# Optimization experiments

Measured on AMD Instinct MI355X. Metric: run time of the kernel, lower is better.

## Reference

```python
import jax, jax.numpy as jnp
import numpy as np

B, T, E, H = 2, 2048, 1024, 16
D = E // H  # head_dim = 64


def setup_inputs() -> dict:
    key = jax.random.key(0)
    kx, kq, kk, kv, ko = jax.random.split(key, 5)
    x = jax.random.normal(kx, (B, T, E), dtype=jnp.float32)
    # nn.Parameter(torch.randn(...)) -> standard normal params
    Wq = jax.random.normal(kq, (H, E, D), dtype=jnp.float32)
    Wk = jax.random.normal(kk, (H, E, D), dtype=jnp.float32)
    Wv = jax.random.normal(kv, (H, E, D), dtype=jnp.float32)
    # nn.Linear(E, E, bias=False): weight [out, in], y = a @ Wo.T
    Wo = jax.random.normal(ko, (E, E), dtype=jnp.float32) * (1.0 / np.sqrt(E))
    # boolean mask: True positions are filled with -inf (causal: strict upper tri)
    mask = jnp.triu(jnp.ones((T, T), dtype=bool), k=1)
    return {"x": x, "mask": mask, "Wq": Wq, "Wk": Wk, "Wv": Wv, "Wo": Wo}


def reference(x, mask, Wq, Wk, Wv, Wo):
    # x: [b, t, e]; Wq/Wk/Wv: [h, e, i]
    q = jnp.einsum('hei,bte->hbti', Wq, x)
    k = jnp.einsum('hei,bte->hbti', Wk, x)
    v = jnp.einsum('hei,bte->hbti', Wv, x)
    # NOTE: original scales by sqrt(seq_len) (x.shape[1]), not sqrt(head_dim)
    scale = x.shape[1] ** 0.5
    fit = jnp.einsum('hbti,hbTi->hbtT', q, k) / scale  # [h, b, t, T]
    fit = jnp.where(mask, -jnp.inf, fit)
    p = jax.nn.softmax(fit, axis=-1)
    att = jnp.einsum('hbtT,hbTi->hbti', p, v)          # [h, b, t, i]
    # rearrange 'h b t i -> b t (h i)'
    b, t = att.shape[1], att.shape[2]
    att = jnp.transpose(att, (1, 2, 0, 3)).reshape(b, t, -1)
    return att @ Wo.T
```

## Files before the change

kernel.cpp:

```cpp
#include <hip/hip_runtime.h>
#include <hip/hip_fp8.h>
#include <stdint.h>

constexpr float INV_SCALE = 0.022097086912079608f;
constexpr float LOG2E = 1.4426950408889634f;
constexpr float QSC = INV_SCALE * LOG2E;

typedef __attribute__((ext_vector_type(8))) short bfrag;
typedef __attribute__((ext_vector_type(4))) float facc;
typedef __attribute__((ext_vector_type(4))) unsigned short us4;

#define MFMA(a, b, c) __builtin_amdgcn_mfma_f32_16x16x32_bf16((a), (b), (c), 0, 0, 0)
#define EXP2(x) __builtin_amdgcn_exp2f(x)

__device__ __forceinline__ unsigned short f2bh(float f) {
    union { float f; unsigned int u; } cv; cv.f = f;
    unsigned int u = cv.u;
    u += 0x7FFFu + ((u >> 16) & 1u);
    return (unsigned short)(u >> 16);
}
__device__ __forceinline__ float bh2f(unsigned short h) {
    union { unsigned int u; float f; } cv; cv.u = ((unsigned int)h) << 16;
    return cv.f;
}
__device__ __forceinline__ void gl_lds16(const unsigned short* g, unsigned short* lds) {
    __builtin_amdgcn_global_load_lds(
        (const __attribute__((address_space(1))) unsigned int*)g,
        (__attribute__((address_space(3))) unsigned int*)lds, 16, 0, 0);
}
__device__ __forceinline__ bfrag f8frag(uint2 raw) {
    union { uint2 u; unsigned char b[8]; } cv; cv.u = raw;
    bfrag r;
    #pragma unroll
    for (int j = 0; j < 8; ++j) {
        const __hip_fp8_e4m3* t = reinterpret_cast<const __hip_fp8_e4m3*>(&cv.b[j]);
        r[j] = (short)f2bh((float)(*t) * 0.00390625f);
    }
    return r;
}

__global__ __launch_bounds__(256) void prep_xw(const float* __restrict__ x,
                                               const float* __restrict__ Wo,
                                               unsigned short* __restrict__ xh,
                                               unsigned short* __restrict__ xl,
                                               unsigned short* __restrict__ WoB) {
    if (blockIdx.x < 1024) {
        int idx = blockIdx.x * 256 + threadIdx.x;
        facc v = *(const facc*)&Wo[(size_t)idx * 4];
        us4 o;
        #pragma unroll
        for (int j = 0; j < 4; ++j) o[j] = f2bh(v[j]);
        *(us4*)&WoB[(size_t)idx * 4] = o;
    } else {
        int idx = (blockIdx.x - 1024) * 256 + threadIdx.x;
        facc v = *(const facc*)&x[(size_t)idx * 4];
        us4 hv, lv;
        #pragma unroll
        for (int j = 0; j < 4; ++j) {
            unsigned short hb = f2bh(v[j]);
            hv[j] = hb;
            lv[j] = f2bh(v[j] - bh2f(hb));
        }
        *(us4*)&xh[(size_t)idx * 4] = hv;
        *(us4*)&xl[(size_t)idx * 4] = lv;
    }
}

__global__ __launch_bounds__(256) void prep_w(
    const float* __restrict__ Wq, const float* __restrict__ Wk, const float* __restrict__ Wv,
    unsigned short* __restrict__ WqTh, unsigned short* __restrict__ WqTl,
    unsigned short* __restrict__ WkTh, unsigned short* __restrict__ WkTl,
    unsigned short* __restrict__ WvT)
{
    __shared__ float tile[64][65];
    const int tid = threadIdx.x;
    const int et = blockIdx.x, h = blockIdx.y, m = blockIdx.z;
    const float* W = (m == 0) ? Wq : (m == 1) ? Wk : Wv;
    #pragma unroll
    for (int rep = 0; rep < 4; ++rep) {
        int idx = rep * 256 + tid;
        int e = idx >> 4, i4 = (idx & 15) * 4;
        facc v = *(const facc*)&W[(size_t)h * 65536 + (size_t)(et * 64 + e) * 64 + i4];
        tile[e][i4] = v.x; tile[e][i4 + 1] = v.y; tile[e][i4 + 2] = v.z; tile[e][i4 + 3] = v.w;
    }
    __syncthreads();
    unsigned short* Oh = (m == 0) ? WqTh : (m == 1) ? WkTh : WvT;
    unsigned short* Ol = (m == 0) ? WqTl : WkTl;
    #pragma unroll
    for (int rep = 0; rep < 4; ++rep) {
        int idx = rep * 256 + tid;
        int i = idx >> 4, e4 = (idx & 15) * 4;
        us4 hv, lv;
        #pragma unroll
        for (int j = 0; j < 4; ++j) {
            float f = tile[e4 + j][i];
            unsigned short hb = f2bh(f);
            hv[j] = hb;
            lv[j] = f2bh(f - bh2f(hb));
        }
        size_t o = (size_t)(h * 64 + i) * 1024 + et * 64 + e4;
        *(us4*)&Oh[o] = hv;
        if (m < 2) *(us4*)&Ol[o] = lv;
    }
}

__global__ __launch_bounds__(512, 2) void qkv_fused(
    const unsigned short* __restrict__ xh, const unsigned short* __restrict__ xl,
    const unsigned short* __restrict__ WqTh, const unsigned short* __restrict__ WqTl,
    const unsigned short* __restrict__ WkTh, const unsigned short* __restrict__ WkTl,
    const unsigned short* __restrict__ WvT,
    unsigned short* __restrict__ qh, unsigned char* __restrict__ ql8,
    unsigned short* __restrict__ kh, unsigned short* __restrict__ kl,
    unsigned short* __restrict__ vT)
{
    extern __shared__ unsigned short sm[];
    unsigned short* Ab = sm;
    unsigned short* Qb = sm + 16384;
    unsigned short* Kb = sm + 32768;
    unsigned short* Vb = sm + 49152;
    const int tid = threadIdx.x;
    const int w = tid >> 6, l = tid & 63;
    const int wm = w >> 2, wn = w & 3;
    const int ct = blockIdx.x, rt = blockIdx.y;

    const int lc = (l & 7) ^ (l >> 3);
    const int krel = (lc & 3) * 8;
    const unsigned short* Axp = (lc < 4) ? xh : xl;
    const unsigned short* Qp  = (lc < 4) ? WqTh : WqTl;
    const unsigned short* Kp  = (lc < 4) ? WkTh : WkTl;

    facc accq[4][2], acck[4][2], accv[4][2];
    #pragma unroll
    for (int m = 0; m < 4; ++m)
        #pragma unroll
        for (int n = 0; n < 2; ++n) {
            accq[m][n] = (facc)(0.0f); acck[m][n] = (facc)(0.0f); accv[m][n] = (facc)(0.0f);
        }

    auto stageAB = [&](int buf, int e0) {
        #pragma unroll
        for (int i = 0; i < 2; ++i) {
            int slice = w * 2 + i;
            int row = slice * 8 + (l >> 3);
            size_t sa = (size_t)(rt * 128 + row) * 1024 + e0 + krel;
            size_t sb = (size_t)(ct * 128 + row) * 1024 + e0 + krel;
            gl_lds16(&Axp[sa], &Ab[buf * 8192 + slice * 512]);
            gl_lds16(&Qp[sb],  &Qb[buf * 8192 + slice * 512]);
            gl_lds16(&Kp[sb],  &Kb[buf * 8192 + slice * 512]);
        }
    };

    stageAB(0, 0);
    #pragma unroll
    for (int i = 0; i < 2; ++i) {
        int slice = w * 2 + i;
        int row = slice * 8 + (l >> 3);
        gl_lds16(&WvT[(size_t)(ct * 128 + row) * 1024 + lc * 8], &Vb[slice * 512]);
    }
    asm volatile("s_waitcnt vmcnt(0)" ::: "memory");
    __builtin_amdgcn_s_barrier();

    for (int t = 0; t < 32; ++t) {
        __builtin_amdgcn_s_barrier();
        __builtin_amdgcn_sched_barrier(0);
        if (t < 31) stageAB((t + 1) & 1, (t + 1) * 32);
        {
            int wv = (t >> 1) + 1;
            if (wv < 16) {
                int slice = w + (t & 1) * 8;
                int row = slice * 8 + (l >> 3);
                gl_lds16(&WvT[(size_t)(ct * 128 + row) * 1024 + wv * 64 + lc * 8],
                         &Vb[(wv & 1) * 8192 + slice * 512]);
            }
        }
        __builtin_amdgcn_sched_barrier(0);
        if (t < 30)       asm volatile("s_waitcnt vmcnt(7)" ::: "memory");
        else if (t == 30) asm volatile("s_waitcnt vmcnt(6)" ::: "memory");
        else              asm volatile("s_waitcnt vmcnt(0)" ::: "memory");
        __builtin_amdgcn_sched_barrier(0);
        __builtin_amdgcn_s_barrier();
        __builtin_amdgcn_sched_barrier(0);

        const unsigned short* Ac = &Ab[(t & 1) * 8192];
        const unsigned short* Qc = &Qb[(t & 1) * 8192];
        const unsigned short* Kc = &Kb[(t & 1) * 8192];
        const unsigned short* Vc = &Vb[((t >> 1) & 1) * 8192];
        const int ca = (l >> 4) ^ (l & 7);
        const int cb = ca ^ 4;
        const int cv = ca ^ ((t & 1) << 2);

        bfrag afh[4], afl[4];
        #pragma unroll
        for (int m = 0; m < 4; ++m) {
            int row = wm * 64 + m * 16 + (l & 15);
            afh[m] = *(const bfrag*)&Ac[row * 64 + ca * 8];
            afl[m] = *(const bfrag*)&Ac[row * 64 + cb * 8];
        }
        #pragma unroll
        for (int n = 0; n < 2; ++n) {
            int nr = wn * 32 + n * 16 + (l & 15);
            bfrag bv = *(const bfrag*)&Vc[nr * 64 + cv * 8];
            #pragma unroll
            for (int m = 0; m < 4; ++m) accv[m][n] = MFMA(afh[m], bv, accv[m][n]);
        }
        #pragma unroll
        for (int n = 0; n < 2; ++n) {
            int nr = wn * 32 + n * 16 + (l & 15);
            bfrag bh = *(const bfrag*)&Qc[nr * 64 + ca * 8];
            bfrag bl = *(const bfrag*)&Qc[nr * 64 + cb * 8];
            #pragma unroll
            for (int m = 0; m < 4; ++m) {
                accq[m][n] = MFMA(afh[m], bh, accq[m][n]);
                accq[m][n] = MFMA(afh[m], bl, accq[m][n]);
                accq[m][n] = MFMA(afl[m], bh, accq[m][n]);
            }
        }
        #pragma unroll
        for (int n = 0; n < 2; ++n) {
            int nr = wn * 32 + n * 16 + (l & 15);
            bfrag bh = *(const bfrag*)&Kc[nr * 64 + ca * 8];
            bfrag bl = *(const bfrag*)&Kc[nr * 64 + cb * 8];
            #pragma unroll
            for (int m = 0; m < 4; ++m) {
                acck[m][n] = MFMA(afh[m], bh, acck[m][n]);
                acck[m][n] = MFMA(afh[m], bl, acck[m][n]);
                acck[m][n] = MFMA(afl[m], bh, acck[m][n]);
            }
        }
    }

    #pragma unroll
    for (int m = 0; m < 4; ++m)
        #pragma unroll
        for (int r = 0; r < 4; ++r) {
            int row = rt * 128 + wm * 64 + m * 16 + (l >> 4) * 4 + r;
            #pragma unroll
            for (int n = 0; n < 2; ++n) {
                int col = ct * 128 + wn * 32 + n * 16 + (l & 15);
                float fq = accq[m][n][r] * QSC;
                unsigned short hb = f2bh(fq);
                qh[(size_t)row * 1024 + col] = hb;
                __hip_fp8_e4m3 e((fq - bh2f(hb)) * 256.0f);
                ql8[(size_t)row * 1024 + col] = *reinterpret_cast<unsigned char*>(&e);
                float fk = acck[m][n][r];
                unsigned short kb = f2bh(fk);
                kh[(size_t)row * 1024 + col] = kb;
                kl[(size_t)row * 1024 + col] = f2bh(fk - bh2f(kb));
            }
        }
    #pragma unroll
    for (int m = 0; m < 4; ++m) {
        int t0g = rt * 128 + wm * 64 + m * 16 + (l >> 4) * 4;
        int b_ = t0g >> 11, t0 = t0g & 2047;
        #pragma unroll
        for (int n = 0; n < 2; ++n) {
            int col = ct * 128 + wn * 32 + n * 16 + (l & 15);
            int h_ = col >> 6, d = col & 63;
            us4 pk;
            #pragma unroll
            for (int r = 0; r < 4; ++r) pk[r] = f2bh(accv[m][n][r]);
            *(us4*)&vT[((size_t)((h_ * 2 + b_) * 64 + d)) * 2048 + t0] = pk;
        }
    }
}

__device__ __forceinline__ void stage_kv(
    const unsigned short* __restrict__ kh, const unsigned short* __restrict__ kl,
    const unsigned short* __restrict__ vT,
    unsigned short* Khb, unsigned short* Klb, unsigned short* Vtb,
    int w, int l, int b, int h, int kt)
{
    #pragma unroll
    for (int i = 0; i < 2; ++i) {
        int pbase = (w * 2 + i) * 1024;
        int p = pbase + l * 16;
        int row = p >> 7, slot = (p >> 4) & 7;
        int chunk = slot ^ (row & 7);
        size_t srcK = (size_t)(b * 2048 + kt * 64 + row) * 1024 + h * 64 + chunk * 8;
        size_t srcV = ((size_t)(h * 2 + b) * 64 + row) * 2048 + (size_t)kt * 64 + chunk * 8;
        gl_lds16(&kh[srcK], &Khb[pbase >> 1]);
        gl_lds16(&kl[srcK], &Klb[pbase >> 1]);
        gl_lds16(&vT[srcV], &Vtb[pbase >> 1]);
    }
}

__device__ __forceinline__ void causal_mask(facc* S, int w, int l) {
    #pragma unroll
    for (int f = 0; f < 4; ++f) {
        int keyl = f * 16 + (l & 15);
        #pragma unroll
        for (int r = 0; r < 4; ++r) {
            int qls = w * 16 + (l >> 4) * 4 + r;
            if (keyl > qls) S[f][r] = -1e30f;
        }
    }
}

__device__ __forceinline__ void softmax_pw(
    facc* S, float* mrow, float* lrow, facc* O,
    unsigned short* Pl, int w, int l)
{
    float mx[4];
    float dmax = -3.0e38f;
    #pragma unroll
    for (int r = 0; r < 4; ++r) {
        float m0 = fmaxf(fmaxf(S[0][r], S[1][r]), fmaxf(S[2][r], S[3][r]));
        m0 = fmaxf(m0, __shfl_xor(m0, 1));
        m0 = fmaxf(m0, __shfl_xor(m0, 2));
        m0 = fmaxf(m0, __shfl_xor(m0, 4));
        m0 = fmaxf(m0, __shfl_xor(m0, 8));
        mx[r] = m0;
        dmax = fmaxf(dmax, m0 - mrow[r]);
    }
    if (!__all(dmax <= 8.0f)) {
        #pragma unroll
        for (int r = 0; r < 4; ++r) {
            float mn = fmaxf(mrow[r], mx[r]);
            float fac = EXP2(mrow[r] - mn);
            mrow[r] = mn;
            lrow[r] *= fac;
            O[0][r] *= fac; O[1][r] *= fac; O[2][r] *= fac; O[3][r] *= fac;
        }
    }
    #pragma unroll
    for (int r = 0; r < 4; ++r) {
        float rs = 0.0f;
        #pragma unroll
        for (int f = 0; f < 4; ++f) { S[f][r] = EXP2(S[f][r] - mrow[r]); rs += S[f][r]; }
        rs += __shfl_xor(rs, 1); rs += __shfl_xor(rs, 2);
        rs += __shfl_xor(rs, 4); rs += __shfl_xor(rs, 8);
        lrow[r] += rs;
    }
    #pragma unroll
    for (int f = 0; f < 4; ++f) {
        int key = f * 16 + (l & 15);
        #pragma unroll
        for (int r = 0; r < 4; ++r) {
            int qr = w * 16 + (l >> 4) * 4 + r;
            Pl[qr * 64 + (((key >> 3) ^ (qr & 7)) * 8) + (key & 7)] = f2bh(S[f][r]);
        }
    }
}

__global__ __launch_bounds__(256, 2) void attn_mfma(
    const unsigned short* __restrict__ qh, const unsigned char* __restrict__ ql8,
    const unsigned short* __restrict__ kh, const unsigned short* __restrict__ kl,
    const unsigned short* __restrict__ vT, unsigned short* __restrict__ att)
{
    extern __shared__ unsigned short smA[];
    unsigned short* Kh = smA;
    unsigned short* Kl = smA + 8192;
    unsigned short* Vt = smA + 16384;
    unsigned short* PlA = smA + 24576;
    unsigned short* PlB = smA + 28672;
    const int tid = threadIdx.x, w = tid >> 6, l = tid & 63;
    const int dd = blockIdx.y * 16 + blockIdx.x;
    const int xcd = dd & 7, sl = dd >> 3;
    const int hb = xcd * 4 + (sl >> 4);
    const int bx = sl & 15;
    const int qtA = 31 - bx, qtB = bx;
    const int h = hb >> 1, b = hb & 1;

    bfrag qfhA[2], qflA[2], qfhB[2], qflB[2];
    {
        const int qrowA = qtA * 64 + w * 16 + (l & 15);
        const size_t qoffA = (size_t)(b * 2048 + qrowA) * 1024 + h * 64 + (l >> 4) * 8;
        qfhA[0] = *(const bfrag*)&qh[qoffA];
        qfhA[1] = *(const bfrag*)&qh[qoffA + 32];
        qflA[0] = f8frag(*(const uint2*)&ql8[qoffA]);
        qflA[1] = f8frag(*(const uint2*)&ql8[qoffA + 32]);
        const int qrowB = qtB * 64 + w * 16 + (l & 15);
        const size_t qoffB = (size_t)(b * 2048 + qrowB) * 1024 + h * 64 + (l >> 4) * 8;
        qfhB[0] = *(const bfrag*)&qh[qoffB];
        qfhB[1] = *(const bfrag*)&qh[qoffB + 32];
        qflB[0] = f8frag(*(const uint2*)&ql8[qoffB]);
        qflB[1] = f8frag(*(const uint2*)&ql8[qoffB + 32]);
    }

    facc OA[4], OB[4];
    float mA[4], lA[4], mB[4], lB[4];
    #pragma unroll
    for (int f = 0; f < 4; ++f) { OA[f] = (facc)(0.0f); OB[f] = (facc)(0.0f); }
    #pragma unroll
    for (int r = 0; r < 4; ++r) { mA[r] = -1e30f; lA[r] = 0.0f; mB[r] = -1e30f; lB[r] = 0.0f; }

    stage_kv(kh, kl, vT, Kh, Kl, Vt, w, l, b, h, 0);
    for (int kt = 0; kt <= qtA; ++kt) {
        const int cur = kt & 1;
        __syncthreads();
        if (kt < qtA)
            stage_kv(kh, kl, vT, &Kh[(cur ^ 1) * 4096], &Kl[(cur ^ 1) * 4096],
                     &Vt[(cur ^ 1) * 4096], w, l, b, h, kt + 1);
        __builtin_amdgcn_sched_barrier(0);
        __builtin_amdgcn_s_barrier();
        __builtin_amdgcn_sched_barrier(0);

        const unsigned short* Khc = &Kh[cur * 4096];
        const unsigned short* Klc = &Kl[cur * 4096];
        const unsigned short* Vtc = &Vt[cur * 4096];

        if (kt <= qtB) {
            facc SA[4], SB[4];
            #pragma unroll
            for (int f = 0; f < 4; ++f) { SA[f] = (facc)(0.0f); SB[f] = (facc)(0.0f); }
            #pragma unroll
            for (int s = 0; s < 2; ++s) {
                #pragma unroll
                for (int f = 0; f < 4; ++f) {
                    int key = f * 16 + (l & 15);
                    int ch = (s * 4 + (l >> 4)) ^ (key & 7);
                    bfrag kbh = *(const bfrag*)&Khc[key * 64 + ch * 8];
                    bfrag kbl = *(const bfrag*)&Klc[key * 64 + ch * 8];
                    SA[f] = MFMA(qfhA[s], kbh, SA[f]);
                    SA[f] = MFMA(qfhA[s], kbl, SA[f]);
                    SA[f] = MFMA(qflA[s], kbh, SA[f]);
                    SB[f] = MFMA(qfhB[s], kbh, SB[f]);
                    SB[f] = MFMA(qfhB[s], kbl, SB[f]);
                    SB[f] = MFMA(qflB[s], kbh, SB[f]);
                }
            }
            if (kt == qtB) causal_mask(SB, w, l);
            softmax_pw(SA, mA, lA, OA, PlA, w, l);
            softmax_pw(SB, mB, lB, OB, PlB, w, l);
            #pragma unroll
            for (int s = 0; s < 2; ++s) {
                int qa = w * 16 + (l & 15);
                int cha = (s * 4 + (l >> 4)) ^ (qa & 7);
                bfrag paA = *(const bfrag*)&PlA[qa * 64 + cha * 8];
                bfrag paB = *(const bfrag*)&PlB[qa * 64 + cha * 8];
                #pragma unroll
                for (int f = 0; f < 4; ++f) {
                    int d = f * 16 + (l & 15);
                    int chv = (s * 4 + (l >> 4)) ^ (d & 7);
                    bfrag vb = *(const bfrag*)&Vtc[d * 64 + chv * 8];
                    OA[f] = MFMA(paA, vb, OA[f]);
                    OB[f] = MFMA(paB, vb, OB[f]);
                }
            }
        } else {
            facc S[4];
            #pragma unroll
            for (int f = 0; f < 4; ++f) S[f] = (facc)(0.0f);
            #pragma unroll
            for (int s = 0; s < 2; ++s) {
                #pragma unroll
                for (int f = 0; f < 4; ++f) {
                    int key = f * 16 + (l & 15);
                    int ch = (s * 4 + (l >> 4)) ^ (key & 7);
                    bfrag kbh = *(const bfrag*)&Khc[key * 64 + ch * 8];
                    bfrag kbl = *(const bfrag*)&Klc[key * 64 + ch * 8];
                    S[f] = MFMA(qfhA[s], kbh, S[f]);
                    S[f] = MFMA(qfhA[s], kbl, S[f]);
                    S[f] = MFMA(qflA[s], kbh, S[f]);
                }
            }
            if (kt == qtA) causal_mask(S, w, l);
            softmax_pw(S, mA, lA, OA, PlA, w, l);
            #pragma unroll
            for (int s = 0; s < 2; ++s) {
                int qa = w * 16 + (l & 15);
                int cha = (s * 4 + (l >> 4)) ^ (qa & 7);
                bfrag pa = *(const bfrag*)&PlA[qa * 64 + cha * 8];
                #pragma unroll
                for (int f = 0; f < 4; ++f) {
                    int d = f * 16 + (l & 15);
                    int chv = (s * 4 + (l >> 4)) ^ (d & 7);
                    bfrag vb = *(const bfrag*)&Vtc[d * 64 + chv * 8];
                    OA[f] = MFMA(pa, vb, OA[f]);
                }
            }
        }
    }

    #pragma unroll
    for (int f = 0; f < 4; ++f) {
        int d = h * 64 + f * 16 + (l & 15);
        #pragma unroll
        for (int r = 0; r < 4; ++r) {
            int tA = qtA * 64 + w * 16 + (l >> 4) * 4 + r;
            att[(size_t)(b * 2048 + tA) * 1024 + d] = f2bh(OA[f][r] / lA[r]);
            int tB = qtB * 64 + w * 16 + (l >> 4) * 4 + r;
            att[(size_t)(b * 2048 + tB) * 1024 + d] = f2bh(OB[f][r] / lB[r]);
        }
    }
}

__global__ __launch_bounds__(256, 2) void outproj(
    const unsigned short* __restrict__ att, const unsigned short* __restrict__ WoB,
    float* __restrict__ out)
{
    __shared__ unsigned short Ab[2][128 * 64], Bb[2][128 * 64];
    const int tid = threadIdx.x, w = tid >> 6, l = tid & 63;
    const int wm = w >> 1, wn = w & 1;
    const int rt = blockIdx.x, ct = blockIdx.y;

    const int lc = (l & 7) ^ (l >> 3);
    facc acc[4][4];
    #pragma unroll
    for (int i = 0; i < 4; ++i)
        #pragma unroll
        for (int j = 0; j < 4; ++j) acc[i][j] = (facc)(0.0f);

    auto stage = [&](int buf, int e0) {
        #pragma unroll
        for (int i = 0; i < 4; ++i) {
            int slice = w * 4 + i;
            int row = slice * 8 + (l >> 3);
            gl_lds16(&att[(size_t)(rt * 128 + row) * 1024 + e0 + lc * 8], &Ab[buf][slice * 512]);
            gl_lds16(&WoB[(size_t)(ct * 128 + row) * 1024 + e0 + lc * 8], &Bb[buf][slice * 512]);
        }
    };

    stage(0, 0);
    int cur = 0;
    for (int t = 0; t < 16; ++t) {
        __syncthreads();
        if (t < 15) stage(cur ^ 1, (t + 1) * 64);
        __builtin_amdgcn_sched_barrier(0);
        __builtin_amdgcn_s_barrier();
        __builtin_amdgcn_sched_barrier(0);
        #pragma unroll
        for (int s = 0; s < 2; ++s) {
            const int slot = (s * 4 + (l >> 4)) ^ (l & 7);
            bfrag af[4], bf_[4];
            #pragma unroll
            for (int m = 0; m < 4; ++m)
                af[m] = *(const bfrag*)&Ab[cur][(wm * 64 + m * 16 + (l & 15)) * 64 + slot * 8];
            #pragma unroll
            for (int n = 0; n < 4; ++n)
                bf_[n] = *(const bfrag*)&Bb[cur][(wn * 64 + n * 16 + (l & 15)) * 64 + slot * 8];
            #pragma unroll
            for (int m = 0; m < 4; ++m)
                #pragma unroll
                for (int n = 0; n < 4; ++n)
                    acc[m][n] = MFMA(af[m], bf_[n], acc[m][n]);
        }
        cur ^= 1;
    }
    #pragma unroll
    for (int m = 0; m < 4; ++m)
        #pragma unroll
        for (int r = 0; r < 4; ++r) {
            int row = rt * 128 + wm * 64 + m * 16 + (l >> 4) * 4 + r;
            #pragma unroll
            for (int n = 0; n < 4; ++n) {
                int col = ct * 128 + wn * 64 + n * 16 + (l & 15);
                out[(size_t)row * 1024 + col] = acc[m][n][r];
            }
        }
}

extern "C" void kernel_launch(void* const* d_in, const int* in_sizes, int n_in,
                              void* d_out, int out_size, void* d_ws, size_t ws_size,
                              hipStream_t stream) {
    const float* x  = (const float*)d_in[0];
    const float* Wq = (const float*)d_in[2];
    const float* Wk = (const float*)d_in[3];
    const float* Wv = (const float*)d_in[4];
    const float* Wo = (const float*)d_in[5];

    uint8_t* wsb = (uint8_t*)d_ws;
    const size_t MB = 1024 * 1024;
    unsigned short* WqTh = (unsigned short*)(wsb + 0 * MB);
    unsigned short* WqTl = (unsigned short*)(wsb + 2 * MB);
    unsigned short* WkTh = (unsigned short*)(wsb + 4 * MB);
    unsigned short* WkTl = (unsigned short*)(wsb + 6 * MB);
    unsigned short* WvT  = (unsigned short*)(wsb + 8 * MB);
    unsigned short* qh   = (unsigned short*)(wsb + 10 * MB);
    unsigned char*  ql8  = (unsigned char*)(wsb + 18 * MB);
    unsigned short* kh   = (unsigned short*)(wsb + 22 * MB);
    unsigned short* kl   = (unsigned short*)(wsb + 30 * MB);
    unsigned short* vT   = (unsigned short*)(wsb + 38 * MB);
    unsigned short* att  = (unsigned short*)(wsb + 46 * MB);
    unsigned short* xh   = (unsigned short*)(wsb + 46 * MB);
    unsigned short* WoB  = (unsigned short*)(wsb + 54 * MB);
    unsigned short* xl   = (unsigned short*)(wsb + 56 * MB);

    hipFuncSetAttribute((const void*)qkv_fused,
                        hipFuncAttributeMaxDynamicSharedMemorySize, 131072);
    hipFuncSetAttribute((const void*)attn_mfma,
                        hipFuncAttributeMaxDynamicSharedMemorySize, 65536);

    prep_xw<<<dim3(5120), 256, 0, stream>>>(x, Wo, xh, xl, WoB);
    prep_w<<<dim3(16, 16, 3), 256, 0, stream>>>(Wq, Wk, Wv, WqTh, WqTl, WkTh, WkTl, WvT);
    qkv_fused<<<dim3(8, 32), 512, 131072, stream>>>(xh, xl, WqTh, WqTl, WkTh, WkTl, WvT,
                                                    qh, ql8, kh, kl, vT);
    attn_mfma<<<dim3(16, 32), 256, 65536, stream>>>(qh, ql8, kh, kl, vT, att);
    outproj<<<dim3(32, 8), 256, 0, stream>>>(att, WoB, (float*)d_out);
}
```

Measured before the change: 180.5 us.

## Software-pipeline QK^T with register-resident fragment-layout V and MFMA row sums

The QKV kernel now writes V in a pre-swizzled MFMA fragment layout, so the attention kernel loads V fragments straight from global memory into registers and no longer stages them in LDS. The attention loop is software-pipelined: the QK^T scores for the next key tile are computed before the softmax and PV of the current tile, with K double-buffered two tiles ahead. The softmax row-sum shuffles are replaced by an extra MFMA against a ones vector. A single shared P buffer is reused for both query tiles, which cuts LDS use. The cost is more live registers for two score sets plus eight V fragments, which could cause spills, and uncached global V loads on the critical path.

```diff
diff --git a/kernel.cpp b/kernel.cpp
--- a/kernel.cpp
+++ b/kernel.cpp
@@ -111,7 +111,7 @@
     const unsigned short* __restrict__ WvT,
     unsigned short* __restrict__ qh, unsigned char* __restrict__ ql8,
     unsigned short* __restrict__ kh, unsigned short* __restrict__ kl,
-    unsigned short* __restrict__ vT)
+    unsigned short* __restrict__ vF)
 {
     extern __shared__ unsigned short sm[];
     unsigned short* Ab = sm;
@@ -252,23 +252,27 @@
     for (int m = 0; m < 4; ++m) {
         int t0g = rt * 128 + wm * 64 + m * 16 + (l >> 4) * 4;
         int b_ = t0g >> 11, t0 = t0g & 2047;
+        int kt = t0 >> 6, tin = t0 & 63;
+        int c = tin >> 3, s = c >> 2;
         #pragma unroll
         for (int n = 0; n < 2; ++n) {
             int col = ct * 128 + wn * 32 + n * 16 + (l & 15);
             int h_ = col >> 6, d = col & 63;
+            int f = d >> 4;
+            int lane_v = (d & 15) | ((c & 3) << 4);
             us4 pk;
             #pragma unroll
             for (int r = 0; r < 4; ++r) pk[r] = f2bh(accv[m][n][r]);
-            *(us4*)&vT[((size_t)((h_ * 2 + b_) * 64 + d)) * 2048 + t0] = pk;
-        }
-    }
-}
-
-__device__ __forceinline__ void stage_kv(
+            size_t off = (((size_t)(h_ * 2 + b_) * 32 + kt) * 8 + s * 4 + f) * 512
+                         + lane_v * 8 + (tin & 7);
+            *(us4*)&vF[off] = pk;
+        }
+    }
+}
+
+__device__ __forceinline__ void stage_k(
     const unsigned short* __restrict__ kh, const unsigned short* __restrict__ kl,
-    const unsigned short* __restrict__ vT,
-    unsigned short* Khb, unsigned short* Klb, unsigned short* Vtb,
-    int w, int l, int b, int h, int kt)
+    unsigned short* Khb, unsigned short* Klb, int w, int l, int b, int h, int kt)
 {
     #pragma unroll
     for (int i = 0; i < 2; ++i) {
@@ -277,10 +281,29 @@
         int row = p >> 7, slot = (p >> 4) & 7;
         int chunk = slot ^ (row & 7);
         size_t srcK = (size_t)(b * 2048 + kt * 64 + row) * 1024 + h * 64 + chunk * 8;
-        size_t srcV = ((size_t)(h * 2 + b) * 64 + row) * 2048 + (size_t)kt * 64 + chunk * 8;
         gl_lds16(&kh[srcK], &Khb[pbase >> 1]);
         gl_lds16(&kl[srcK], &Klb[pbase >> 1]);
-        gl_lds16(&vT[srcV], &Vtb[pbase >> 1]);
+    }
+}
+
+__device__ __forceinline__ void qkt_tile(
+    const unsigned short* Khc, const unsigned short* Klc,
+    const bfrag* qfh, const bfrag* qfl, facc* S, int l)
+{
+    #pragma unroll
+    for (int f = 0; f < 4; ++f) S[f] = (facc)(0.0f);
+    #pragma unroll
+    for (int s = 0; s < 2; ++s) {
+        #pragma unroll
+        for (int f = 0; f < 4; ++f) {
+            int key = f * 16 + (l & 15);
+            int ch = (s * 4 + (l >> 4)) ^ (key & 7);
+            bfrag kbh = *(const bfrag*)&Khc[key * 64 + ch * 8];
+            bfrag kbl = *(const bfrag*)&Klc[key * 64 + ch * 8];
+            S[f] = MFMA(qfh[s], kbh, S[f]);
+            S[f] = MFMA(qfh[s], kbl, S[f]);
+            S[f] = MFMA(qfl[s], kbh, S[f]);
+        }
     }
 }
 
@@ -297,8 +320,7 @@
 }
 
 __device__ __forceinline__ void softmax_pw(
-    facc* S, float* mrow, float* lrow, facc* O,
-    unsigned short* Pl, int w, int l)
+    facc* S, float* mrow, facc* O, facc& Osum, unsigned short* Pl, int w, int l)
 {
     float mx[4];
     float dmax = -3.0e38f;
@@ -318,19 +340,14 @@
             float mn = fmaxf(mrow[r], mx[r]);
             float fac = EXP2(mrow[r] - mn);
             mrow[r] = mn;
-            lrow[r] *= fac;
             O[0][r] *= fac; O[1][r] *= fac; O[2][r] *= fac; O[3][r] *= fac;
-        }
-    }
-    #pragma unroll
-    for (int r = 0; r < 4; ++r) {
-        float rs = 0.0f;
-        #pragma unroll
-        for (int f = 0; f < 4; ++f) { S[f][r] = EXP2(S[f][r] - mrow[r]); rs += S[f][r]; }
-        rs += __shfl_xor(rs, 1); rs += __shfl_xor(rs, 2);
-        rs += __shfl_xor(rs, 4); rs += __shfl_xor(rs, 8);
-        lrow[r] += rs;
-    }
+            Osum[r] *= fac;
+        }
+    }
+    #pragma unroll
+    for (int r = 0; r < 4; ++r)
+        #pragma unroll
+        for (int f = 0; f < 4; ++f) S[f][r] = EXP2(S[f][r] - mrow[r]);
     #pragma unroll
     for (int f = 0; f < 4; ++f) {
         int key = f * 16 + (l & 15);
@@ -342,17 +359,28 @@
     }
 }
 
+__device__ __forceinline__ void pv(
+    const bfrag* vf, const unsigned short* Pl, facc* O, facc& Osum,
+    bfrag ones, int w, int l)
+{
+    #pragma unroll
+    for (int s = 0; s < 2; ++s) {
+        int qa = w * 16 + (l & 15);
+        int cha = (s * 4 + (l >> 4)) ^ (qa & 7);
+        bfrag pa = *(const bfrag*)&Pl[qa * 64 + cha * 8];
+        Osum = MFMA(pa, ones, Osum);
+        #pragma unroll
+        for (int f = 0; f < 4; ++f)
+            O[f] = MFMA(pa, vf[s * 4 + f], O[f]);
+    }
+}
+
 __global__ __launch_bounds__(256, 2) void attn_mfma(
     const unsigned short* __restrict__ qh, const unsigned char* __restrict__ ql8,
     const unsigned short* __restrict__ kh, const unsigned short* __restrict__ kl,
-    const unsigned short* __restrict__ vT, unsigned short* __restrict__ att)
-{
-    extern __shared__ unsigned short smA[];
-    unsigned short* Kh = smA;
-    unsigned short* Kl = smA + 8192;
-    unsigned short* Vt = smA + 16384;
-    unsigned short* PlA = smA + 24576;
-    unsigned short* PlB = smA + 28672;
+    const unsigned short* __restrict__ vF, unsigned short* __restrict__ att)
+{
+    __shared__ unsigned short Kh[2][4096], Kl[2][4096], Pl[4096];
     const int tid = threadIdx.x, w = tid >> 6, l = tid & 63;
     const int dd = blockIdx.y * 16 + blockIdx.x;
     const int xcd = dd & 7, sl = dd >> 3;
@@ -360,6 +388,11 @@
     const int bx = sl & 15;
     const int qtA = 31 - bx, qtB = bx;
     const int h = hb >> 1, b = hb & 1;
+    const unsigned short* vFb = vF + (size_t)hb * 32 * 8 * 512;
+
+    bfrag ones;
+    #pragma unroll
+    for (int j = 0; j < 8; ++j) ones[j] = (short)0x3F80;
 
     bfrag qfhA[2], qflA[2], qfhB[2], qflB[2];
     {
@@ -377,99 +410,53 @@
         qflB[1] = f8frag(*(const uint2*)&ql8[qoffB + 32]);
     }
 
-    facc OA[4], OB[4];
-    float mA[4], lA[4], mB[4], lB[4];
+    facc OA[4], OB[4], OsA, OsB;
+    float mA[4], mB[4];
     #pragma unroll
     for (int f = 0; f < 4; ++f) { OA[f] = (facc)(0.0f); OB[f] = (facc)(0.0f); }
-    #pragma unroll
-    for (int r = 0; r < 4; ++r) { mA[r] = -1e30f; lA[r] = 0.0f; mB[r] = -1e30f; lB[r] = 0.0f; }
-
-    stage_kv(kh, kl, vT, Kh, Kl, Vt, w, l, b, h, 0);
+    OsA = (facc)(0.0f); OsB = (facc)(0.0f);
+    #pragma unroll
+    for (int r = 0; r < 4; ++r) { mA[r] = -1e30f; mB[r] = -1e30f; }
+
+    facc S0A[4], S0B[4], S1A[4], S1B[4];
+
+    stage_k(kh, kl, Kh[0], Kl[0], w, l, b, h, 0);
+    stage_k(kh, kl, Kh[1], Kl[1], w, l, b, h, 1);
+    __syncthreads();
+    qkt_tile(Kh[0], Kl[0], qfhA, qflA, S0A, l);
+    qkt_tile(Kh[0], Kl[0], qfhB, qflB, S0B, l);
+    if (qtB == 0) causal_mask(S0B, w, l);
+
+    auto step = [&](int kt, facc* ScA, facc* ScB, facc* SnA, facc* SnB) {
+        __syncthreads();
+        bfrag vf[8];
+        {
+            const unsigned short* vb = vFb + (size_t)kt * 4096 + l * 8;
+            #pragma unroll
+            for (int i = 0; i < 8; ++i)
+                vf[i] = *(const bfrag*)&vb[i * 512];
+        }
+        if (kt + 2 <= qtA)
+            stage_k(kh, kl, Kh[kt & 1], Kl[kt & 1], w, l, b, h, kt + 2);
+        if (kt + 1 <= qtA) {
+            qkt_tile(Kh[(kt + 1) & 1], Kl[(kt + 1) & 1], qfhA, qflA, SnA, l);
+            if (kt + 1 == qtA) causal_mask(SnA, w, l);
+        }
+        if (kt + 1 <= qtB) {
+            qkt_tile(Kh[(kt + 1) & 1], Kl[(kt + 1) & 1], qfhB, qflB, SnB, l);
+            if (kt + 1 == qtB) causal_mask(SnB, w, l);
+        }
+        softmax_pw(ScA, mA, OA, OsA, Pl, w, l);
+        pv(vf, Pl, OA, OsA, ones, w, l);
+        if (kt <= qtB) {
+            softmax_pw(ScB, mB, OB, OsB, Pl, w, l);
+            pv(vf, Pl, OB, OsB, ones, w, l);
+        }
+    };
+
     for (int kt = 0; kt <= qtA; ++kt) {
-        const int cur = kt & 1;
-        __syncthreads();
-        if (kt < qtA)
-            stage_kv(kh, kl, vT, &Kh[(cur ^ 1) * 4096], &Kl[(cur ^ 1) * 4096],
-                     &Vt[(cur ^ 1) * 4096], w, l, b, h, kt + 1);
-        __builtin_amdgcn_sched_barrier(0);
-        __builtin_amdgcn_s_barrier();
-        __builtin_amdgcn_sched_barrier(0);
-
-        const unsigned short* Khc = &Kh[cur * 4096];
-        const unsigned short* Klc = &Kl[cur * 4096];
-        const unsigned short* Vtc = &Vt[cur * 4096];
-
-        if (kt <= qtB) {
-            facc SA[4], SB[4];
-            #pragma unroll
-            for (int f = 0; f < 4; ++f) { SA[f] = (facc)(0.0f); SB[f] = (facc)(0.0f); }
-            #pragma unroll
-            for (int s = 0; s < 2; ++s) {
-                #pragma unroll
-                for (int f = 0; f < 4; ++f) {
-                    int key = f * 16 + (l & 15);
-                    int ch = (s * 4 + (l >> 4)) ^ (key & 7);
-                    bfrag kbh = *(const bfrag*)&Khc[key * 64 + ch * 8];
-                    bfrag kbl = *(const bfrag*)&Klc[key * 64 + ch * 8];
-                    SA[f] = MFMA(qfhA[s], kbh, SA[f]);
-                    SA[f] = MFMA(qfhA[s], kbl, SA[f]);
-                    SA[f] = MFMA(qflA[s], kbh, SA[f]);
-                    SB[f] = MFMA(qfhB[s], kbh, SB[f]);
-                    SB[f] = MFMA(qfhB[s], kbl, SB[f]);
-                    SB[f] = MFMA(qflB[s], kbh, SB[f]);
-                }
-            }
-            if (kt == qtB) causal_mask(SB, w, l);
-            softmax_pw(SA, mA, lA, OA, PlA, w, l);
-            softmax_pw(SB, mB, lB, OB, PlB, w, l);
-            #pragma unroll
-            for (int s = 0; s < 2; ++s) {
-                int qa = w * 16 + (l & 15);
-                int cha = (s * 4 + (l >> 4)) ^ (qa & 7);
-                bfrag paA = *(const bfrag*)&PlA[qa * 64 + cha * 8];
-                bfrag paB = *(const bfrag*)&PlB[qa * 64 + cha * 8];
-                #pragma unroll
-                for (int f = 0; f < 4; ++f) {
-                    int d = f * 16 + (l & 15);
-                    int chv = (s * 4 + (l >> 4)) ^ (d & 7);
-                    bfrag vb = *(const bfrag*)&Vtc[d * 64 + chv * 8];
-                    OA[f] = MFMA(paA, vb, OA[f]);
-                    OB[f] = MFMA(paB, vb, OB[f]);
-                }
-            }
-        } else {
-            facc S[4];
-            #pragma unroll
-            for (int f = 0; f < 4; ++f) S[f] = (facc)(0.0f);
-            #pragma unroll
-            for (int s = 0; s < 2; ++s) {
-                #pragma unroll
-                for (int f = 0; f < 4; ++f) {
-                    int key = f * 16 + (l & 15);
-                    int ch = (s * 4 + (l >> 4)) ^ (key & 7);
-                    bfrag kbh = *(const bfrag*)&Khc[key * 64 + ch * 8];
-                    bfrag kbl = *(const bfrag*)&Klc[key * 64 + ch * 8];
-                    S[f] = MFMA(qfhA[s], kbh, S[f]);
-                    S[f] = MFMA(qfhA[s], kbl, S[f]);
-                    S[f] = MFMA(qflA[s], kbh, S[f]);
-                }
-            }
-            if (kt == qtA) causal_mask(S, w, l);
-            softmax_pw(S, mA, lA, OA, PlA, w, l);
-            #pragma unroll
-            for (int s = 0; s < 2; ++s) {
-                int qa = w * 16 + (l & 15);
-                int cha = (s * 4 + (l >> 4)) ^ (qa & 7);
-                bfrag pa = *(const bfrag*)&PlA[qa * 64 + cha * 8];
-                #pragma unroll
-                for (int f = 0; f < 4; ++f) {
-                    int d = f * 16 + (l & 15);
-                    int chv = (s * 4 + (l >> 4)) ^ (d & 7);
-                    bfrag vb = *(const bfrag*)&Vtc[d * 64 + chv * 8];
-                    OA[f] = MFMA(pa, vb, OA[f]);
-                }
-            }
-        }
+        if (kt & 1) step(kt, S1A, S1B, S0A, S0B);
+        else        step(kt, S0A, S0B, S1A, S1B);
     }
 
     #pragma unroll
@@ -478,9 +465,9 @@
         #pragma unroll
         for (int r = 0; r < 4; ++r) {
             int tA = qtA * 64 + w * 16 + (l >> 4) * 4 + r;
-            att[(size_t)(b * 2048 + tA) * 1024 + d] = f2bh(OA[f][r] / lA[r]);
+            att[(size_t)(b * 2048 + tA) * 1024 + d] = f2bh(OA[f][r] / OsA[r]);
             int tB = qtB * 64 + w * 16 + (l >> 4) * 4 + r;
-            att[(size_t)(b * 2048 + tB) * 1024 + d] = f2bh(OB[f][r] / lB[r]);
+            att[(size_t)(b * 2048 + tB) * 1024 + d] = f2bh(OB[f][r] / OsB[r]);
         }
     }
 }
@@ -570,7 +557,7 @@
     unsigned char*  ql8  = (unsigned char*)(wsb + 18 * MB);
     unsigned short* kh   = (unsigned short*)(wsb + 22 * MB);
     unsigned short* kl   = (unsigned short*)(wsb + 30 * MB);
-    unsigned short* vT   = (unsigned short*)(wsb + 38 * MB);
+    unsigned short* vF   = (unsigned short*)(wsb + 38 * MB);
     unsigned short* att  = (unsigned short*)(wsb + 46 * MB);
     unsigned short* xh   = (unsigned short*)(wsb + 46 * MB);
     unsigned short* WoB  = (unsigned short*)(wsb + 54 * MB);
@@ -578,13 +565,11 @@
 
     hipFuncSetAttribute((const void*)qkv_fused,
                         hipFuncAttributeMaxDynamicSharedMemorySize, 131072);
-    hipFuncSetAttribute((const void*)attn_mfma,
-                        hipFuncAttributeMaxDynamicSharedMemorySize, 65536);
 
     prep_xw<<<dim3(5120), 256, 0, stream>>>(x, Wo, xh, xl, WoB);
     prep_w<<<dim3(16, 16, 3), 256, 0, stream>>>(Wq, Wk, Wv, WqTh, WqTl, WkTh, WkTl, WvT);
     qkv_fused<<<dim3(8, 32), 512, 131072, stream>>>(xh, xl, WqTh, WqTl, WkTh, WkTl, WvT,
-                                                    qh, ql8, kh, kl, vT);
-    attn_mfma<<<dim3(16, 32), 256, 65536, stream>>>(qh, ql8, kh, kl, vT, att);
+                                                    qh, ql8, kh, kl, vF);
+    attn_mfma<<<dim3(16, 32), 256, 0, stream>>>(qh, ql8, kh, kl, vF, att);
     outproj<<<dim3(32, 8), 256, 0, stream>>>(att, WoB, (float*)d_out);
 }
```

Result: slower. 394.8 us (+118.8%).
